# Kernel tuning notes

Measured on AMD Instinct MI355X. Metric: run time of the kernel, lower is better.

## Reference

```python
import jax, jax.numpy as jnp
import numpy as np

B, T, F, H, L, C = 32, 512, 1024, 1024, 2, 2
W_SCALE = 0.03  # small init so tanh stays in its linear-ish range


def setup_inputs() -> dict:
    key = jax.random.key(0)
    ks = jax.random.split(key, 12)
    inp = {
        "x": jax.random.normal(ks[0], (B, T, F), dtype=jnp.float32),
        "h0": jax.random.normal(ks[1], (L, B, H), dtype=jnp.float32),
        # layer 0 (input size F)
        "W_ih0": jax.random.normal(ks[2], (H, F), dtype=jnp.float32) * W_SCALE,
        "W_hh0": jax.random.normal(ks[3], (H, H), dtype=jnp.float32) * W_SCALE,
        "b_ih0": jax.random.normal(ks[4], (H,), dtype=jnp.float32) * W_SCALE,
        "b_hh0": jax.random.normal(ks[5], (H,), dtype=jnp.float32) * W_SCALE,
        # layer 1 (input size H)
        "W_ih1": jax.random.normal(ks[6], (H, H), dtype=jnp.float32) * W_SCALE,
        "W_hh1": jax.random.normal(ks[7], (H, H), dtype=jnp.float32) * W_SCALE,
        "b_ih1": jax.random.normal(ks[8], (H,), dtype=jnp.float32) * W_SCALE,
        "b_hh1": jax.random.normal(ks[9], (H,), dtype=jnp.float32) * W_SCALE,
        # classifier Linear(T*H -> C)
        "W_cls": jax.random.normal(ks[10], (C, T * H), dtype=jnp.float32) * 0.001,
        "b_cls": jax.random.normal(ks[11], (C,), dtype=jnp.float32) * 0.001,
    }
    return inp


def _rnn_layer(x_btf, h0_bh, W_ih, W_hh, b_ih, b_hh):
    # PyTorch RNN (tanh): h_t = tanh(x_t W_ih^T + b_ih + h_{t-1} W_hh^T + b_hh)
    # Precompute the input projection for all timesteps (one big GEMM).
    pre = jnp.einsum("btf,hf->bth", x_btf, W_ih) + b_ih + b_hh  # [B,T,H]
    pre_t = jnp.swapaxes(pre, 0, 1)  # [T,B,H] for scan

    def step(h, p):  # h: [B,H], p: [B,H]
        h_new = jnp.tanh(p + h @ W_hh.T)
        return h_new, h_new

    h_last, ys = jax.lax.scan(step, h0_bh, pre_t)
    return jnp.swapaxes(ys, 0, 1), h_last  # [B,T,H], [B,H]


def reference(x, h0, W_ih0, W_hh0, b_ih0, b_hh0, W_ih1, W_hh1, b_ih1, b_hh1, W_cls, b_cls):
    y0, h0_last = _rnn_layer(x, h0[0], W_ih0, W_hh0, b_ih0, b_hh0)
    y1, h1_last = _rnn_layer(y0, h0[1], W_ih1, W_hh1, b_ih1, b_hh1)
    h_n = jnp.stack([h0_last, h1_last], axis=0)  # [L,B,H]
    flat = y1.reshape(y1.shape[0], -1)  # [B, T*H]
    logits = flat @ W_cls.T + b_cls  # Dropout(0.1) is identity at inference
    return logits, h_n
```

## Files before the change

### kernel.cpp

```cpp
#include <hip/hip_runtime.h>
#include <math.h>

typedef float f4 __attribute__((ext_vector_type(4)));
typedef short bf16x8 __attribute__((ext_vector_type(8)));
typedef unsigned u32x2 __attribute__((ext_vector_type(2)));
typedef unsigned u32x4 __attribute__((ext_vector_type(4)));

#define NT 512

#define H00 0
#define H01 32768
#define H10 65536
#define H11 98304
#define PLOG 131072
#define FLAGS 135168
#define WSW  139520
#define XBF  4333824

__device__ __forceinline__ unsigned pack_bf16(float lo, float hi) {
  unsigned u;
  asm volatile("v_cvt_pk_bf16_f32 %0, %1, %2" : "=v"(u) : "v"(lo), "v"(hi));
  return u;
}
__device__ __forceinline__ float bflo(unsigned d) { return __uint_as_float(d << 16); }
__device__ __forceinline__ float bfhi(unsigned d) { return __uint_as_float(d & 0xffff0000u); }
__device__ __forceinline__ void st_cohf(float* p, float v) {
  __hip_atomic_store(p, v, __ATOMIC_RELAXED, __HIP_MEMORY_SCOPE_AGENT);
}
__device__ __forceinline__ void st_cohu(unsigned* p, unsigned v) {
  __hip_atomic_store(p, v, __ATOMIC_RELAXED, __HIP_MEMORY_SCOPE_AGENT);
}
__device__ __forceinline__ unsigned ld_flag(const unsigned* p) {
  return __hip_atomic_load(p, __ATOMIC_RELAXED, __HIP_MEMORY_SCOPE_AGENT);
}

__device__ __forceinline__ void split8(const f4 v0, const f4 v1, u32x4& hi, u32x4& lo) {
  float h_[8] = {v0[0], v0[1], v0[2], v0[3], v1[0], v1[1], v1[2], v1[3]};
  #pragma unroll
  for (int e = 0; e < 4; ++e) hi[e] = pack_bf16(h_[2*e], h_[2*e+1]);
  float r[8];
  #pragma unroll
  for (int e = 0; e < 4; ++e) {
    r[2*e]   = h_[2*e]   - bflo(hi[e]);
    r[2*e+1] = h_[2*e+1] - bfhi(hi[e]);
  }
  #pragma unroll
  for (int e = 0; e < 4; ++e) lo[e] = pack_bf16(r[2*e], r[2*e+1]);
}

__global__ __launch_bounds__(128) void wconv_kernel(
    const float* __restrict__ W0, const float* __restrict__ W1,
    const float* __restrict__ W2, const float* __restrict__ W3,
    float* __restrict__ ws) {
  const int mat = blockIdx.x >> 10;
  const int j = blockIdx.x & 1023;
  const int kc = threadIdx.x;
  const float* Wm = (mat == 0) ? W0 : (mat == 1) ? W1 : (mat == 2) ? W2 : W3;
  const f4* src = (const f4*)(Wm + (size_t)j * 1024 + kc * 8);
  f4 v0 = src[0], v1 = src[1];
  u32x4 hi, lo;
  split8(v0, v1, hi, lo);
  u32x4* dst = (u32x4*)((f4*)ws + (WSW >> 2));
  size_t base = (size_t)(mat * 2) * 131072 + (j >> 4) * 2048 + kc * 16 + (j & 15);
  dst[base] = hi;
  dst[base + 131072] = lo;
}

__global__ __launch_bounds__(128) void xconv_kernel(const float* __restrict__ x,
                                                    float* __restrict__ ws) {
  const int t = blockIdx.x;
  const int kc = threadIdx.x;
  u32x4* dst = (u32x4*)((f4*)ws + (XBF >> 2)) + (size_t)t * 4096;
  for (int b = 0; b < 32; ++b) {
    const f4* src = (const f4*)(x + ((size_t)b * NT + t) * 1024 + kc * 8);
    f4 v0 = src[0], v1 = src[1];
    u32x4 p;
    #pragma unroll
    for (int e = 0; e < 4; ++e)
      p[e] = pack_bf16(e < 2 ? v0[2*e] : v1[2*e-4], e < 2 ? v0[2*e+1] : v1[2*e-3]);
    dst[(size_t)kc * 32 + b] = p;
  }
}

__global__ __launch_bounds__(256) void hinit_kernel(const float* __restrict__ h0,
                                                    float* __restrict__ ws) {
  int g = blockIdx.x * 256 + threadIdx.x;
  int l = g >> 12, b = (g >> 7) & 31, kc = g & 127;
  const f4* src = (const f4*)(h0 + (size_t)l * 32768 + b * 1024 + kc * 8);
  f4 v0 = src[0], v1 = src[1];
  u32x4 hi, lo;
  split8(v0, v1, hi, lo);
  u32x4* d = (u32x4*)((unsigned*)ws + (l ? H11 : H00));
  d[(size_t)kc * 32 + b] = hi;
  d[4096 + (size_t)kc * 32 + b] = lo;
  if (g < 4352) ((unsigned*)ws)[FLAGS + g] = 0u;
}

#define LDG(dst, ptr) \
  asm volatile("global_load_dwordx4 %0, %1, off sc0" : "=v"(dst) : "v"(ptr))
#define MFMA(a, b, c) __builtin_amdgcn_mfma_f32_16x16x32_bf16(a, b, c, 0, 0, 0)
#define BC(v) __builtin_bit_cast(bf16x8, v)

#define KT_L0(kt, N)                                                     \
  asm volatile("s_waitcnt vmcnt(" #N ")");                               \
  __builtin_amdgcn_sched_barrier(0xF4);                                  \
  {                                                                      \
    const int ci = (ch0 + kt * 4) * 16 + jl;                             \
    bf16x8 a0 = w4b[ci], a1 = w4b[2048 + ci], a2 = w4b[4096 + ci];       \
    bf16x8 vh = BC(bh[kt]), vl = BC(bl[kt]), vx = BC(bx[kt]);            \
    cr = MFMA(a0, vh, cr); cr = MFMA(a0, vl, cr); cr = MFMA(a1, vh, cr); \
    cp = MFMA(a2, vx, cp);                                               \
  }

#define KT_L1(kt, N)                                                     \
  asm volatile("s_waitcnt vmcnt(" #N ")");                               \
  __builtin_amdgcn_sched_barrier(0xF4);                                  \
  {                                                                      \
    const int ci = (ch0 + kt * 4) * 16 + jl;                             \
    bf16x8 a0 = w4b[ci], a1 = w4b[2048 + ci];                            \
    bf16x8 a2 = w4b[4096 + ci], a3 = w4b[6144 + ci];                     \
    bf16x8 h0h = BC(bh[kt]), h0l = BC(bl[kt]);                           \
    bf16x8 h1h = BC(ch_[kt]), h1l = BC(cl_[kt]);                         \
    cr = MFMA(a0, h0h, cr); cr = MFMA(a0, h0l, cr); cr = MFMA(a1, h0h, cr); \
    cr = MFMA(a2, h1h, cr); cr = MFMA(a2, h1l, cr); cr = MFMA(a3, h1h, cr); \
  }

#define KT_PRE(kt, N)                                                    \
  asm volatile("s_waitcnt vmcnt(" #N ")");                               \
  __builtin_amdgcn_sched_barrier(0xF4);                                  \
  {                                                                      \
    const int ci = (ch0 + kt * 4) * 16 + jl;                             \
    bf16x8 a2 = w4b[4096 + ci];                                          \
    cp = MFMA(a2, BC(bx[kt]), cp);                                       \
  }

__global__ __launch_bounds__(512, 1) void rnn_kernel(
    const float* __restrict__ bih0, const float* __restrict__ bhh0,
    const float* __restrict__ bih1, const float* __restrict__ bhh1,
    const float* __restrict__ Wcls, const float* __restrict__ bcls,
    float* __restrict__ out, float* ws) {
  extern __shared__ float smem[];
  f4* w4 = (f4*)smem;
  bf16x8* w4b = (bf16x8*)smem;
  f4* partR = w4 + 8192;
  f4* partP = w4 + 8704;
  float* prebuf = smem + 36864;

  const int bid = blockIdx.x, tid = threadIdx.x;
  const bool isL1 = bid >= 64;
  const int jsl = bid & 63;
  const int l = tid & 63, w = tid >> 6;
  const int nt = w & 1, ks = w >> 1;
  const int jl = l & 15;
  const int bcol = nt * 16 + (l & 15);
  const int ch0 = ks * 32 + (l >> 4);

  unsigned* flags = (unsigned*)ws + FLAGS;
  unsigned* relc = flags + 4096;
  const f4* wsf4 = (const f4*)ws;

  {
    const int m0 = isL1 ? 2 : 0;
    for (int i = tid; i < 8192; i += 512) {
      const int slot = i >> 11, idx = i & 2047;
      const int mat = m0 + (slot >> 1), part = slot & 1;
      w4[i] = wsf4[(WSW >> 2) + (size_t)(mat * 2 + part) * 131072 +
                   jsl * 2048 + idx];
    }
  }

  const int rr = tid & 63, ntr = (tid >> 6) & 1;
  const int b_r = ntr * 16 + (rr & 15);
  const int jg = rr >> 4;
  const int jcol0 = jsl * 16 + jg * 4;
  f4 biasv = (f4)0.f;
  if (tid < 128) {
    f4 bi = isL1 ? *(const f4*)(bih1 + jcol0) : *(const f4*)(bih0 + jcol0);
    f4 bh2 = isL1 ? *(const f4*)(bhh1 + jcol0) : *(const f4*)(bhh0 + jcol0);
    biasv = bi + bh2;
  }
  float lg0 = 0.f, lg1 = 0.f;
  __syncthreads();

  if (!isL1) {
    f4 bx[8];
    const f4* px = wsf4 + (XBF >> 2) + ch0 * 32 + bcol;
    LDG(bx[0], px);            LDG(bx[1], px + 128);
    LDG(bx[2], px + 256);      LDG(bx[3], px + 384);
    LDG(bx[4], px + 512);      LDG(bx[5], px + 640);
    LDG(bx[6], px + 768);      LDG(bx[7], px + 896);
    f4 cp = (f4)0.f;
    KT_PRE(0, 7) KT_PRE(1, 6) KT_PRE(2, 5) KT_PRE(3, 4)
    KT_PRE(4, 3) KT_PRE(5, 2) KT_PRE(6, 1) KT_PRE(7, 0)
    partP[(ks * 2 + nt) * 64 + l] = cp;
    __syncthreads();
    if (tid >= 128 && tid < 256) {
      f4 sum = partP[ntr * 64 + rr] + partP[(2 + ntr) * 64 + rr] +
               partP[(4 + ntr) * 64 + rr] + partP[(6 + ntr) * 64 + rr];
      #pragma unroll
      for (int e = 0; e < 4; ++e)
        prebuf[(jg * 4 + e) * 32 + b_r] = sum[e];
    }
    __syncthreads();
  }

  for (int s = 0; s <= NT; ++s) {
    if (bid == 0) {
      if (tid < 128) {
        const unsigned* fp = &flags[tid * 32];
        while (ld_flag(fp) < (unsigned)s) {}
      }
      __syncthreads();
      if (tid < 8) st_cohu(&relc[tid * 32], (unsigned)s);
    } else {
      if (tid == 0) {
        const unsigned* rxp = &relc[(bid & 7) * 32];
        while (ld_flag(rxp) < (unsigned)s) {}
      }
      __syncthreads();
    }
    __builtin_amdgcn_sched_barrier(0);

    const int rp = s & 1;
    const bool act = isL1 ? (s >= 1) : (s < NT);

    f4 wc0 = (f4)0.f, wc1 = (f4)0.f;
    if (isL1 && tid < 128 && s >= 1) {
      wc0 = *(const f4*)(Wcls + (size_t)(s - 1) * 1024 + jcol0);
      wc1 = *(const f4*)(Wcls + (size_t)524288 + (size_t)(s - 1) * 1024 + jcol0);
    }

    if (act) {
      if (!isL1) {
        const int tn = (s + 1 < NT) ? (s + 1) : (NT - 1);
        const f4* ph = wsf4 + ((rp ? H01 : H00) >> 2) + ch0 * 32 + bcol;
        const f4* pl = ph + 4096;
        const f4* px = wsf4 + (XBF >> 2) + (size_t)tn * 4096 + ch0 * 32 + bcol;
        f4 bh[8], bl[8], bx[8];
        LDG(bh[0], ph);       LDG(bl[0], pl);       LDG(bx[0], px);
        LDG(bh[1], ph + 128); LDG(bl[1], pl + 128); LDG(bx[1], px + 128);
        LDG(bh[2], ph + 256); LDG(bl[2], pl + 256); LDG(bx[2], px + 256);
        LDG(bh[3], ph + 384); LDG(bl[3], pl + 384); LDG(bx[3], px + 384);
        LDG(bh[4], ph + 512); LDG(bl[4], pl + 512); LDG(bx[4], px + 512);
        LDG(bh[5], ph + 640); LDG(bl[5], pl + 640); LDG(bx[5], px + 640);
        LDG(bh[6], ph + 768); LDG(bl[6], pl + 768); LDG(bx[6], px + 768);
        LDG(bh[7], ph + 896); LDG(bl[7], pl + 896); LDG(bx[7], px + 896);
        f4 cr = (f4)0.f, cp = (f4)0.f;
        KT_L0(0, 21) KT_L0(1, 18) KT_L0(2, 15) KT_L0(3, 12)
        KT_L0(4, 9)  KT_L0(5, 6)  KT_L0(6, 3)  KT_L0(7, 0)
        partR[(ks * 2 + nt) * 64 + l] = cr;
        partP[(ks * 2 + nt) * 64 + l] = cp;
      } else {
        const f4* ph = wsf4 + ((rp ? H01 : H00) >> 2) + ch0 * 32 + bcol;
        const f4* pl = ph + 4096;
        const f4* qh = wsf4 + ((rp ? H11 : H10) >> 2) + ch0 * 32 + bcol;
        const f4* ql = qh + 4096;
        f4 bh[8], bl[8], ch_[8], cl_[8];
        LDG(bh[0], ph);       LDG(bl[0], pl);       LDG(ch_[0], qh);       LDG(cl_[0], ql);
        LDG(bh[1], ph + 128); LDG(bl[1], pl + 128); LDG(ch_[1], qh + 128); LDG(cl_[1], ql + 128);
        LDG(bh[2], ph + 256); LDG(bl[2], pl + 256); LDG(ch_[2], qh + 256); LDG(cl_[2], ql + 256);
        LDG(bh[3], ph + 384); LDG(bl[3], pl + 384); LDG(ch_[3], qh + 384); LDG(cl_[3], ql + 384);
        LDG(bh[4], ph + 512); LDG(bl[4], pl + 512); LDG(ch_[4], qh + 512); LDG(cl_[4], ql + 512);
        LDG(bh[5], ph + 640); LDG(bl[5], pl + 640); LDG(ch_[5], qh + 640); LDG(cl_[5], ql + 640);
        LDG(bh[6], ph + 768); LDG(bl[6], pl + 768); LDG(ch_[6], qh + 768); LDG(cl_[6], ql + 768);
        LDG(bh[7], ph + 896); LDG(bl[7], pl + 896); LDG(ch_[7], qh + 896); LDG(cl_[7], ql + 896);
        f4 cr = (f4)0.f;
        KT_L1(0, 28) KT_L1(1, 24) KT_L1(2, 20) KT_L1(3, 16)
        KT_L1(4, 12) KT_L1(5, 8)  KT_L1(6, 4)  KT_L1(7, 0)
        partR[(ks * 2 + nt) * 64 + l] = cr;
      }
      __syncthreads();

      if (tid < 128) {
        f4 sum = partR[ntr * 64 + rr] + partR[(2 + ntr) * 64 + rr] +
                 partR[(4 + ntr) * 64 + rr] + partR[(6 + ntr) * 64 + rr];
        float h_[4];
        #pragma unroll
        for (int e = 0; e < 4; ++e) {
          float v = sum[e] + biasv[e];
          if (!isL1) v += prebuf[rp * 512 + (jg * 4 + e) * 32 + b_r];
          h_[e] = tanhf(v);
        }
        unsigned hi0 = pack_bf16(h_[0], h_[1]), hi1 = pack_bf16(h_[2], h_[3]);
        float r0 = h_[0] - bflo(hi0), r1 = h_[1] - bfhi(hi0);
        float r2 = h_[2] - bflo(hi1), r3 = h_[3] - bfhi(hi1);
        unsigned lo0 = pack_bf16(r0, r1), lo1 = pack_bf16(r2, r3);
        u32x2 hp; hp[0] = hi0; hp[1] = hi1;
        u32x2 lp; lp[0] = lo0; lp[1] = lo1;
        unsigned dstb = isL1 ? (rp ? H10 : H11) : (rp ? H00 : H01);
        unsigned* dp = (unsigned*)ws + dstb + ((jcol0 >> 3) * 32 + b_r) * 4 +
                       ((jcol0 >> 1) & 3);
        asm volatile("global_store_dwordx2 %0, %1, off sc0 sc1" ::"v"(dp), "v"(hp) : "memory");
        asm volatile("global_store_dwordx2 %0, %1, off sc0 sc1" ::"v"(dp + 16384), "v"(lp) : "memory");
        if (isL1) {
          lg0 += h_[0]*wc0[0] + h_[1]*wc0[1] + h_[2]*wc0[2] + h_[3]*wc0[3];
          lg1 += h_[0]*wc1[0] + h_[1]*wc1[1] + h_[2]*wc1[2] + h_[3]*wc1[3];
          if (s == NT) {
            f4 o; o[0]=h_[0]; o[1]=h_[1]; o[2]=h_[2]; o[3]=h_[3];
            *(f4*)(out + 64 + 32768 + (size_t)b_r * 1024 + jcol0) = o;
          }
        } else if (s == NT - 1) {
          f4 o; o[0]=h_[0]; o[1]=h_[1]; o[2]=h_[2]; o[3]=h_[3];
          *(f4*)(out + 64 + (size_t)b_r * 1024 + jcol0) = o;
        }
      } else if (tid < 256 && !isL1) {
        f4 sum = partP[ntr * 64 + rr] + partP[(2 + ntr) * 64 + rr] +
                 partP[(4 + ntr) * 64 + rr] + partP[(6 + ntr) * 64 + rr];
        #pragma unroll
        for (int e = 0; e < 4; ++e)
          prebuf[(rp ^ 1) * 512 + (jg * 4 + e) * 32 + b_r] = sum[e];
      }
    }
    asm volatile("s_waitcnt vmcnt(0)");
    __syncthreads();
    if (tid == 0) st_cohu(&flags[bid * 32], (unsigned)(s + 1));
  }

  if (isL1) {
    float* lgred = smem + 36864;
    if (tid < 128) {
      lgred[jg * 32 + b_r] = lg0;
      lgred[128 + jg * 32 + b_r] = lg1;
    }
    __syncthreads();
    if (tid < 64) {
      const int c = tid >> 5, bb = tid & 31;
      float v = 0.f;
      #pragma unroll
      for (int g2 = 0; g2 < 4; ++g2) v += lgred[c * 128 + g2 * 32 + bb];
      st_cohf(&ws[PLOG + (size_t)(bid - 64) * 64 + c * 32 + bb], v);
    }
    __syncthreads();
    if (tid == 0) st_cohu(&flags[bid * 32], 600u);
  } else if (bid == 0) {
    if (tid < 64) {
      const unsigned* fp = &flags[(64 + tid) * 32];
      while (ld_flag(fp) < 600u) {}
    }
    __syncthreads();
    __builtin_amdgcn_sched_barrier(0);
    float* lgred = smem + 36864;
    if (tid < 256) {
      const int g2 = tid >> 6, pair = tid & 63;
      float v = 0.f;
      for (int blk = g2; blk < 64; blk += 4)
        v += __hip_atomic_load(&ws[PLOG + (size_t)blk * 64 + pair],
                               __ATOMIC_RELAXED, __HIP_MEMORY_SCOPE_AGENT);
      lgred[tid] = v;
    }
    __syncthreads();
    if (tid < 64) {
      float s2 = bcls[tid >> 5];
      #pragma unroll
      for (int g2 = 0; g2 < 4; ++g2) s2 += lgred[g2 * 64 + tid];
      out[(size_t)(tid & 31) * 2 + (tid >> 5)] = s2;
    }
  }
}

extern "C" void kernel_launch(void* const* d_in, const int* in_sizes, int n_in,
                              void* d_out, int out_size, void* d_ws, size_t ws_size,
                              hipStream_t stream) {
  const float* x    = (const float*)d_in[0];
  const float* h0   = (const float*)d_in[1];
  const float* Wih0 = (const float*)d_in[2];
  const float* Whh0 = (const float*)d_in[3];
  const float* bih0 = (const float*)d_in[4];
  const float* bhh0 = (const float*)d_in[5];
  const float* Wih1 = (const float*)d_in[6];
  const float* Whh1 = (const float*)d_in[7];
  const float* bih1 = (const float*)d_in[8];
  const float* bhh1 = (const float*)d_in[9];
  const float* Wcls = (const float*)d_in[10];
  const float* bcls = (const float*)d_in[11];
  float* out = (float*)d_out;
  float* ws  = (float*)d_ws;

  hipFuncSetAttribute((const void*)rnn_kernel,
                      hipFuncAttributeMaxDynamicSharedMemorySize, 151552);

  hipLaunchKernelGGL(wconv_kernel, dim3(4096), dim3(128), 0, stream,
                     Whh0, Wih0, Wih1, Whh1, ws);
  hipLaunchKernelGGL(xconv_kernel, dim3(512), dim3(128), 0, stream, x, ws);
  hipLaunchKernelGGL(hinit_kernel, dim3(32), dim3(256), 0, stream, h0, ws);

  void* args[] = { (void*)&bih0, (void*)&bhh0, (void*)&bih1, (void*)&bhh1,
                   (void*)&Wcls, (void*)&bcls, (void*)&out, (void*)&ws };
  hipLaunchCooperativeKernel((void*)rnn_kernel, dim3(128), dim3(512), args,
                             151552, stream);
}
```

Baseline: 2.702 ms.

## Decouple RNN layers with per-layer flags and ring-buffered hidden states

Replaces the global per-step barrier (block 0 gathering all flags and broadcasting a release counter) with separate per-layer flag arrays, so layer-0 blocks wait only on their peers and on layer 1 lagging at most three steps. Layer-0 hidden states go into a four-slot ring, and layer 1 now computes its input projection from layer-0 output with split-bf16 MFMAs instead of fusing that work into one step. The x projection for the next step is moved after the flag publish to take it off the critical path. This lets the two layers run pipelined rather than in lockstep, at the cost of more flag polling and a more complex dependency scheme.

```diff
diff --git a/kernel.cpp b/kernel.cpp
--- a/kernel.cpp
+++ b/kernel.cpp
@@ -8,14 +8,12 @@
 
 #define NT 512
 
-#define H00 0
-#define H01 32768
-#define H10 65536
-#define H11 98304
-#define PLOG 131072
-#define FLAGS 135168
-#define WSW  139520
-#define XBF  4333824
+#define H0R 0
+#define H1R 131072
+#define PLOG 196608
+#define FLAGS 200704
+#define WSW 204800
+#define XBF 4399104
 
 __device__ __forceinline__ unsigned pack_bf16(float lo, float hi) {
   unsigned u;
@@ -30,8 +28,8 @@
 __device__ __forceinline__ void st_cohu(unsigned* p, unsigned v) {
   __hip_atomic_store(p, v, __ATOMIC_RELAXED, __HIP_MEMORY_SCOPE_AGENT);
 }
-__device__ __forceinline__ unsigned ld_flag(const unsigned* p) {
-  return __hip_atomic_load(p, __ATOMIC_RELAXED, __HIP_MEMORY_SCOPE_AGENT);
+__device__ __forceinline__ int ld_flag(const unsigned* p) {
+  return (int)__hip_atomic_load(p, __ATOMIC_RELAXED, __HIP_MEMORY_SCOPE_AGENT);
 }
 
 __device__ __forceinline__ void split8(const f4 v0, const f4 v1, u32x4& hi, u32x4& lo) {
@@ -90,10 +88,11 @@
   f4 v0 = src[0], v1 = src[1];
   u32x4 hi, lo;
   split8(v0, v1, hi, lo);
-  u32x4* d = (u32x4*)((unsigned*)ws + (l ? H11 : H00));
+  unsigned base = l ? (H1R + 32768) : (H0R + 3 * 32768);
+  u32x4* d = (u32x4*)((unsigned*)ws + base);
   d[(size_t)kc * 32 + b] = hi;
   d[4096 + (size_t)kc * 32 + b] = lo;
-  if (g < 4352) ((unsigned*)ws)[FLAGS + g] = 0u;
+  if (g < 4096) ((unsigned*)ws)[FLAGS + g] = 0u;
 }
 
 #define LDG(dst, ptr) \
@@ -101,38 +100,44 @@
 #define MFMA(a, b, c) __builtin_amdgcn_mfma_f32_16x16x32_bf16(a, b, c, 0, 0, 0)
 #define BC(v) __builtin_bit_cast(bf16x8, v)
 
-#define KT_L0(kt, N)                                                     \
-  asm volatile("s_waitcnt vmcnt(" #N ")");                               \
-  __builtin_amdgcn_sched_barrier(0xF4);                                  \
-  {                                                                      \
-    const int ci = (ch0 + kt * 4) * 16 + jl;                             \
-    bf16x8 a0 = w4b[ci], a1 = w4b[2048 + ci], a2 = w4b[4096 + ci];       \
-    bf16x8 vh = BC(bh[kt]), vl = BC(bl[kt]), vx = BC(bx[kt]);            \
-    cr = MFMA(a0, vh, cr); cr = MFMA(a0, vl, cr); cr = MFMA(a1, vh, cr); \
-    cp = MFMA(a2, vx, cp);                                               \
-  }
-
-#define KT_L1(kt, N)                                                     \
-  asm volatile("s_waitcnt vmcnt(" #N ")");                               \
-  __builtin_amdgcn_sched_barrier(0xF4);                                  \
-  {                                                                      \
-    const int ci = (ch0 + kt * 4) * 16 + jl;                             \
-    bf16x8 a0 = w4b[ci], a1 = w4b[2048 + ci];                            \
-    bf16x8 a2 = w4b[4096 + ci], a3 = w4b[6144 + ci];                     \
-    bf16x8 h0h = BC(bh[kt]), h0l = BC(bl[kt]);                           \
-    bf16x8 h1h = BC(ch_[kt]), h1l = BC(cl_[kt]);                         \
-    cr = MFMA(a0, h0h, cr); cr = MFMA(a0, h0l, cr); cr = MFMA(a1, h0h, cr); \
-    cr = MFMA(a2, h1h, cr); cr = MFMA(a2, h1l, cr); cr = MFMA(a3, h1h, cr); \
-  }
-
-#define KT_PRE(kt, N)                                                    \
-  asm volatile("s_waitcnt vmcnt(" #N ")");                               \
-  __builtin_amdgcn_sched_barrier(0xF4);                                  \
-  {                                                                      \
-    const int ci = (ch0 + kt * 4) * 16 + jl;                             \
-    bf16x8 a2 = w4b[4096 + ci];                                          \
-    cp = MFMA(a2, BC(bx[kt]), cp);                                       \
-  }
+#define KT_M(kt, N)                                                       \
+  asm volatile("s_waitcnt vmcnt(" #N ")");                                \
+  __builtin_amdgcn_sched_barrier(0xF4);                                   \
+  {                                                                       \
+    const int ci = (ch0 + kt * 4) * 16 + jl;                              \
+    bf16x8 a0 = w4b[ci], a1 = w4b[2048 + ci];                             \
+    bf16x8 vh = BC(bh[kt]), vl = BC(bl[kt]);                              \
+    cr = MFMA(a0, vh, cr); cr = MFMA(a0, vl, cr); cr = MFMA(a1, vh, cr);  \
+  }
+
+#define KT_G(kt, N)                                                       \
+  asm volatile("s_waitcnt vmcnt(" #N ")");                                \
+  __builtin_amdgcn_sched_barrier(0xF4);                                   \
+  {                                                                       \
+    const int ci = (ch0 + kt * 4) * 16 + jl;                              \
+    bf16x8 a2 = w4b[4096 + ci], a3 = w4b[6144 + ci];                      \
+    bf16x8 vh = BC(gh[kt]), vl = BC(gl[kt]);                              \
+    cp = MFMA(a2, vh, cp); cp = MFMA(a2, vl, cp); cp = MFMA(a3, vh, cp);  \
+  }
+
+#define KT_X(kt, N)                                                       \
+  asm volatile("s_waitcnt vmcnt(" #N ")");                                \
+  __builtin_amdgcn_sched_barrier(0xF4);                                   \
+  {                                                                       \
+    const int ci = (ch0 + kt * 4) * 16 + jl;                              \
+    bf16x8 a2 = w4b[4096 + ci];                                           \
+    cp = MFMA(a2, BC(bx[kt]), cp);                                        \
+  }
+
+#define LD16(A, B, pa, pb)                                                \
+  LDG(A[0], pa);       LDG(B[0], pb);                                     \
+  LDG(A[1], pa + 128); LDG(B[1], pb + 128);                               \
+  LDG(A[2], pa + 256); LDG(B[2], pb + 256);                               \
+  LDG(A[3], pa + 384); LDG(B[3], pb + 384);                               \
+  LDG(A[4], pa + 512); LDG(B[4], pb + 512);                               \
+  LDG(A[5], pa + 640); LDG(B[5], pb + 640);                               \
+  LDG(A[6], pa + 768); LDG(B[6], pb + 768);                               \
+  LDG(A[7], pa + 896); LDG(B[7], pb + 896);
 
 __global__ __launch_bounds__(512, 1) void rnn_kernel(
     const float* __restrict__ bih0, const float* __restrict__ bhh0,
@@ -155,17 +160,16 @@
   const int bcol = nt * 16 + (l & 15);
   const int ch0 = ks * 32 + (l >> 4);
 
-  unsigned* flags = (unsigned*)ws + FLAGS;
-  unsigned* relc = flags + 4096;
+  unsigned* flag0 = (unsigned*)ws + FLAGS;
+  unsigned* flag1 = flag0 + 64 * 32;
   const f4* wsf4 = (const f4*)ws;
 
   {
-    const int m0 = isL1 ? 2 : 0;
-    for (int i = tid; i < 8192; i += 512) {
+    const int nent = isL1 ? 8192 : 6144;
+    for (int i = tid; i < nent; i += 512) {
       const int slot = i >> 11, idx = i & 2047;
-      const int mat = m0 + (slot >> 1), part = slot & 1;
-      w4[i] = wsf4[(WSW >> 2) + (size_t)(mat * 2 + part) * 131072 +
-                   jsl * 2048 + idx];
+      const int region = isL1 ? (slot < 2 ? 6 + slot : 2 + slot) : slot;
+      w4[i] = wsf4[(WSW >> 2) + (size_t)region * 131072 + jsl * 2048 + idx];
     }
   }
 
@@ -185,90 +189,54 @@
   if (!isL1) {
     f4 bx[8];
     const f4* px = wsf4 + (XBF >> 2) + ch0 * 32 + bcol;
-    LDG(bx[0], px);            LDG(bx[1], px + 128);
-    LDG(bx[2], px + 256);      LDG(bx[3], px + 384);
-    LDG(bx[4], px + 512);      LDG(bx[5], px + 640);
-    LDG(bx[6], px + 768);      LDG(bx[7], px + 896);
+    LDG(bx[0], px);       LDG(bx[1], px + 128);
+    LDG(bx[2], px + 256); LDG(bx[3], px + 384);
+    LDG(bx[4], px + 512); LDG(bx[5], px + 640);
+    LDG(bx[6], px + 768); LDG(bx[7], px + 896);
     f4 cp = (f4)0.f;
-    KT_PRE(0, 7) KT_PRE(1, 6) KT_PRE(2, 5) KT_PRE(3, 4)
-    KT_PRE(4, 3) KT_PRE(5, 2) KT_PRE(6, 1) KT_PRE(7, 0)
+    KT_X(0, 7) KT_X(1, 6) KT_X(2, 5) KT_X(3, 4)
+    KT_X(4, 3) KT_X(5, 2) KT_X(6, 1) KT_X(7, 0)
     partP[(ks * 2 + nt) * 64 + l] = cp;
-    __syncthreads();
-    if (tid >= 128 && tid < 256) {
-      f4 sum = partP[ntr * 64 + rr] + partP[(2 + ntr) * 64 + rr] +
-               partP[(4 + ntr) * 64 + rr] + partP[(6 + ntr) * 64 + rr];
-      #pragma unroll
-      for (int e = 0; e < 4; ++e)
-        prebuf[(jg * 4 + e) * 32 + b_r] = sum[e];
-    }
-    __syncthreads();
-  }
-
-  for (int s = 0; s <= NT; ++s) {
-    if (bid == 0) {
-      if (tid < 128) {
-        const unsigned* fp = &flags[tid * 32];
-        while (ld_flag(fp) < (unsigned)s) {}
-      }
-      __syncthreads();
-      if (tid < 8) st_cohu(&relc[tid * 32], (unsigned)s);
-    } else {
-      if (tid == 0) {
-        const unsigned* rxp = &relc[(bid & 7) * 32];
-        while (ld_flag(rxp) < (unsigned)s) {}
-      }
-      __syncthreads();
-    }
+  } else {
+    if (tid < 64) { while (ld_flag(&flag0[tid * 32]) < 1) {} }
+    __syncthreads();
     __builtin_amdgcn_sched_barrier(0);
-
-    const int rp = s & 1;
-    const bool act = isL1 ? (s >= 1) : (s < NT);
-
-    f4 wc0 = (f4)0.f, wc1 = (f4)0.f;
-    if (isL1 && tid < 128 && s >= 1) {
-      wc0 = *(const f4*)(Wcls + (size_t)(s - 1) * 1024 + jcol0);
-      wc1 = *(const f4*)(Wcls + (size_t)524288 + (size_t)(s - 1) * 1024 + jcol0);
-    }
-
-    if (act) {
-      if (!isL1) {
-        const int tn = (s + 1 < NT) ? (s + 1) : (NT - 1);
-        const f4* ph = wsf4 + ((rp ? H01 : H00) >> 2) + ch0 * 32 + bcol;
-        const f4* pl = ph + 4096;
-        const f4* px = wsf4 + (XBF >> 2) + (size_t)tn * 4096 + ch0 * 32 + bcol;
-        f4 bh[8], bl[8], bx[8];
-        LDG(bh[0], ph);       LDG(bl[0], pl);       LDG(bx[0], px);
-        LDG(bh[1], ph + 128); LDG(bl[1], pl + 128); LDG(bx[1], px + 128);
-        LDG(bh[2], ph + 256); LDG(bl[2], pl + 256); LDG(bx[2], px + 256);
-        LDG(bh[3], ph + 384); LDG(bl[3], pl + 384); LDG(bx[3], px + 384);
-        LDG(bh[4], ph + 512); LDG(bl[4], pl + 512); LDG(bx[4], px + 512);
-        LDG(bh[5], ph + 640); LDG(bl[5], pl + 640); LDG(bx[5], px + 640);
-        LDG(bh[6], ph + 768); LDG(bl[6], pl + 768); LDG(bx[6], px + 768);
-        LDG(bh[7], ph + 896); LDG(bl[7], pl + 896); LDG(bx[7], px + 896);
-        f4 cr = (f4)0.f, cp = (f4)0.f;
-        KT_L0(0, 21) KT_L0(1, 18) KT_L0(2, 15) KT_L0(3, 12)
-        KT_L0(4, 9)  KT_L0(5, 6)  KT_L0(6, 3)  KT_L0(7, 0)
-        partR[(ks * 2 + nt) * 64 + l] = cr;
-        partP[(ks * 2 + nt) * 64 + l] = cp;
-      } else {
-        const f4* ph = wsf4 + ((rp ? H01 : H00) >> 2) + ch0 * 32 + bcol;
-        const f4* pl = ph + 4096;
-        const f4* qh = wsf4 + ((rp ? H11 : H10) >> 2) + ch0 * 32 + bcol;
-        const f4* ql = qh + 4096;
-        f4 bh[8], bl[8], ch_[8], cl_[8];
-        LDG(bh[0], ph);       LDG(bl[0], pl);       LDG(ch_[0], qh);       LDG(cl_[0], ql);
-        LDG(bh[1], ph + 128); LDG(bl[1], pl + 128); LDG(ch_[1], qh + 128); LDG(cl_[1], ql + 128);
-        LDG(bh[2], ph + 256); LDG(bl[2], pl + 256); LDG(ch_[2], qh + 256); LDG(cl_[2], ql + 256);
-        LDG(bh[3], ph + 384); LDG(bl[3], pl + 384); LDG(ch_[3], qh + 384); LDG(cl_[3], ql + 384);
-        LDG(bh[4], ph + 512); LDG(bl[4], pl + 512); LDG(ch_[4], qh + 512); LDG(cl_[4], ql + 512);
-        LDG(bh[5], ph + 640); LDG(bl[5], pl + 640); LDG(ch_[5], qh + 640); LDG(cl_[5], ql + 640);
-        LDG(bh[6], ph + 768); LDG(bl[6], pl + 768); LDG(ch_[6], qh + 768); LDG(cl_[6], ql + 768);
-        LDG(bh[7], ph + 896); LDG(bl[7], pl + 896); LDG(ch_[7], qh + 896); LDG(cl_[7], ql + 896);
-        f4 cr = (f4)0.f;
-        KT_L1(0, 28) KT_L1(1, 24) KT_L1(2, 20) KT_L1(3, 16)
-        KT_L1(4, 12) KT_L1(5, 8)  KT_L1(6, 4)  KT_L1(7, 0)
-        partR[(ks * 2 + nt) * 64 + l] = cr;
-      }
+    const f4* gph = wsf4 + (H0R >> 2) + ch0 * 32 + bcol;
+    const f4* gpl = gph + 4096;
+    f4 gh[8], gl[8];
+    LD16(gh, gl, gph, gpl)
+    f4 cp = (f4)0.f;
+    KT_G(0, 14) KT_G(1, 12) KT_G(2, 10) KT_G(3, 8)
+    KT_G(4, 6)  KT_G(5, 4)  KT_G(6, 2)  KT_G(7, 0)
+    partP[(ks * 2 + nt) * 64 + l] = cp;
+  }
+  __syncthreads();
+  if (tid >= 128 && tid < 256) {
+    f4 sum = partP[ntr * 64 + rr] + partP[(2 + ntr) * 64 + rr] +
+             partP[(4 + ntr) * 64 + rr] + partP[(6 + ntr) * 64 + rr];
+    #pragma unroll
+    for (int e = 0; e < 4; ++e) prebuf[(jg * 4 + e) * 32 + b_r] = sum[e];
+  }
+
+  if (!isL1) {
+    for (int s = 0; s < NT; ++s) {
+      if (tid < 64) { while (ld_flag(&flag0[tid * 32]) < s) {} }
+      else if (tid < 128) {
+        const int bound = s - 3;
+        while (ld_flag(&flag1[(tid - 64) * 32]) < bound) {}
+      }
+      __syncthreads();
+      __builtin_amdgcn_sched_barrier(0);
+      const int pp = s & 1;
+
+      const f4* ph = wsf4 + (H0R >> 2) + ((s + 3) & 3) * 8192 + ch0 * 32 + bcol;
+      const f4* pl = ph + 4096;
+      f4 bh[8], bl[8];
+      LD16(bh, bl, ph, pl)
+      f4 cr = (f4)0.f;
+      KT_M(0, 14) KT_M(1, 12) KT_M(2, 10) KT_M(3, 8)
+      KT_M(4, 6)  KT_M(5, 4)  KT_M(6, 2)  KT_M(7, 0)
+      partR[(ks * 2 + nt) * 64 + l] = cr;
       __syncthreads();
 
       if (tid < 128) {
@@ -276,48 +244,122 @@
                  partR[(4 + ntr) * 64 + rr] + partR[(6 + ntr) * 64 + rr];
         float h_[4];
         #pragma unroll
-        for (int e = 0; e < 4; ++e) {
-          float v = sum[e] + biasv[e];
-          if (!isL1) v += prebuf[rp * 512 + (jg * 4 + e) * 32 + b_r];
-          h_[e] = tanhf(v);
-        }
+        for (int e = 0; e < 4; ++e)
+          h_[e] = tanhf(sum[e] + biasv[e] + prebuf[pp * 512 + (jg * 4 + e) * 32 + b_r]);
         unsigned hi0 = pack_bf16(h_[0], h_[1]), hi1 = pack_bf16(h_[2], h_[3]);
-        float r0 = h_[0] - bflo(hi0), r1 = h_[1] - bfhi(hi0);
-        float r2 = h_[2] - bflo(hi1), r3 = h_[3] - bfhi(hi1);
-        unsigned lo0 = pack_bf16(r0, r1), lo1 = pack_bf16(r2, r3);
+        unsigned lo0 = pack_bf16(h_[0] - bflo(hi0), h_[1] - bfhi(hi0));
+        unsigned lo1 = pack_bf16(h_[2] - bflo(hi1), h_[3] - bfhi(hi1));
         u32x2 hp; hp[0] = hi0; hp[1] = hi1;
         u32x2 lp; lp[0] = lo0; lp[1] = lo1;
-        unsigned dstb = isL1 ? (rp ? H10 : H11) : (rp ? H00 : H01);
-        unsigned* dp = (unsigned*)ws + dstb + ((jcol0 >> 3) * 32 + b_r) * 4 +
-                       ((jcol0 >> 1) & 3);
+        unsigned* dp = (unsigned*)ws + H0R + (s & 3) * 32768 +
+                       ((jcol0 >> 3) * 32 + b_r) * 4 + ((jcol0 >> 1) & 3);
         asm volatile("global_store_dwordx2 %0, %1, off sc0 sc1" ::"v"(dp), "v"(hp) : "memory");
         asm volatile("global_store_dwordx2 %0, %1, off sc0 sc1" ::"v"(dp + 16384), "v"(lp) : "memory");
-        if (isL1) {
-          lg0 += h_[0]*wc0[0] + h_[1]*wc0[1] + h_[2]*wc0[2] + h_[3]*wc0[3];
-          lg1 += h_[0]*wc1[0] + h_[1]*wc1[1] + h_[2]*wc1[2] + h_[3]*wc1[3];
-          if (s == NT) {
-            f4 o; o[0]=h_[0]; o[1]=h_[1]; o[2]=h_[2]; o[3]=h_[3];
-            *(f4*)(out + 64 + 32768 + (size_t)b_r * 1024 + jcol0) = o;
-          }
-        } else if (s == NT - 1) {
+        if (s == NT - 1) {
           f4 o; o[0]=h_[0]; o[1]=h_[1]; o[2]=h_[2]; o[3]=h_[3];
           *(f4*)(out + 64 + (size_t)b_r * 1024 + jcol0) = o;
         }
-      } else if (tid < 256 && !isL1) {
-        f4 sum = partP[ntr * 64 + rr] + partP[(2 + ntr) * 64 + rr] +
-                 partP[(4 + ntr) * 64 + rr] + partP[(6 + ntr) * 64 + rr];
+      }
+      asm volatile("s_waitcnt vmcnt(0)");
+      __syncthreads();
+      if (tid == 0) st_cohu(&flag0[bid * 32], (unsigned)(s + 1));
+
+      if (s < NT - 1) {
+        const f4* px = wsf4 + (XBF >> 2) + (size_t)(s + 1) * 4096 + ch0 * 32 + bcol;
+        f4 bx[8];
+        LDG(bx[0], px);       LDG(bx[1], px + 128);
+        LDG(bx[2], px + 256); LDG(bx[3], px + 384);
+        LDG(bx[4], px + 512); LDG(bx[5], px + 640);
+        LDG(bx[6], px + 768); LDG(bx[7], px + 896);
+        f4 cp = (f4)0.f;
+        KT_X(0, 7) KT_X(1, 6) KT_X(2, 5) KT_X(3, 4)
+        KT_X(4, 3) KT_X(5, 2) KT_X(6, 1) KT_X(7, 0)
+        partP[(ks * 2 + nt) * 64 + l] = cp;
+        __syncthreads();
+        if (tid >= 128 && tid < 256) {
+          f4 sum = partP[ntr * 64 + rr] + partP[(2 + ntr) * 64 + rr] +
+                   partP[(4 + ntr) * 64 + rr] + partP[(6 + ntr) * 64 + rr];
+          #pragma unroll
+          for (int e = 0; e < 4; ++e)
+            prebuf[(pp ^ 1) * 512 + (jg * 4 + e) * 32 + b_r] = sum[e];
+        }
+      }
+    }
+  } else {
+    for (int t = 0; t < NT; ++t) {
+      if (tid < 64) { while (ld_flag(&flag1[tid * 32]) < t) {} }
+      __syncthreads();
+      __builtin_amdgcn_sched_barrier(0);
+      const int pp = t & 1;
+
+      f4 wc0 = (f4)0.f, wc1 = (f4)0.f;
+      if (tid < 128) {
+        wc0 = *(const f4*)(Wcls + (size_t)t * 1024 + jcol0);
+        wc1 = *(const f4*)(Wcls + (size_t)524288 + (size_t)t * 1024 + jcol0);
+      }
+      __builtin_amdgcn_sched_barrier(0);
+
+      const f4* ph = wsf4 + (H1R >> 2) + ((t + 1) & 1) * 8192 + ch0 * 32 + bcol;
+      const f4* pl = ph + 4096;
+      f4 bh[8], bl[8];
+      LD16(bh, bl, ph, pl)
+      f4 cr = (f4)0.f;
+      KT_M(0, 14) KT_M(1, 12) KT_M(2, 10) KT_M(3, 8)
+      KT_M(4, 6)  KT_M(5, 4)  KT_M(6, 2)  KT_M(7, 0)
+      partR[(ks * 2 + nt) * 64 + l] = cr;
+      __syncthreads();
+
+      if (tid < 128) {
+        f4 sum = partR[ntr * 64 + rr] + partR[(2 + ntr) * 64 + rr] +
+                 partR[(4 + ntr) * 64 + rr] + partR[(6 + ntr) * 64 + rr];
+        float h_[4];
         #pragma unroll
         for (int e = 0; e < 4; ++e)
-          prebuf[(rp ^ 1) * 512 + (jg * 4 + e) * 32 + b_r] = sum[e];
-      }
-    }
-    asm volatile("s_waitcnt vmcnt(0)");
-    __syncthreads();
-    if (tid == 0) st_cohu(&flags[bid * 32], (unsigned)(s + 1));
-  }
-
-  if (isL1) {
-    float* lgred = smem + 36864;
+          h_[e] = tanhf(sum[e] + biasv[e] + prebuf[pp * 512 + (jg * 4 + e) * 32 + b_r]);
+        unsigned hi0 = pack_bf16(h_[0], h_[1]), hi1 = pack_bf16(h_[2], h_[3]);
+        unsigned lo0 = pack_bf16(h_[0] - bflo(hi0), h_[1] - bfhi(hi0));
+        unsigned lo1 = pack_bf16(h_[2] - bflo(hi1), h_[3] - bfhi(hi1));
+        u32x2 hp; hp[0] = hi0; hp[1] = hi1;
+        u32x2 lp; lp[0] = lo0; lp[1] = lo1;
+        unsigned* dp = (unsigned*)ws + H1R + (t & 1) * 32768 +
+                       ((jcol0 >> 3) * 32 + b_r) * 4 + ((jcol0 >> 1) & 3);
+        asm volatile("global_store_dwordx2 %0, %1, off sc0 sc1" ::"v"(dp), "v"(hp) : "memory");
+        asm volatile("global_store_dwordx2 %0, %1, off sc0 sc1" ::"v"(dp + 16384), "v"(lp) : "memory");
+        lg0 += h_[0]*wc0[0] + h_[1]*wc0[1] + h_[2]*wc0[2] + h_[3]*wc0[3];
+        lg1 += h_[0]*wc1[0] + h_[1]*wc1[1] + h_[2]*wc1[2] + h_[3]*wc1[3];
+        if (t == NT - 1) {
+          f4 o; o[0]=h_[0]; o[1]=h_[1]; o[2]=h_[2]; o[3]=h_[3];
+          *(f4*)(out + 64 + 32768 + (size_t)b_r * 1024 + jcol0) = o;
+        }
+      }
+      asm volatile("s_waitcnt vmcnt(0)");
+      __syncthreads();
+      if (tid == 0) st_cohu(&flag1[(bid - 64) * 32], (unsigned)(t + 1));
+
+      if (t < NT - 1) {
+        if (tid < 64) { while (ld_flag(&flag0[tid * 32]) < t + 2) {} }
+        __syncthreads();
+        __builtin_amdgcn_sched_barrier(0);
+        const f4* gph = wsf4 + (H0R >> 2) + ((t + 1) & 3) * 8192 + ch0 * 32 + bcol;
+        const f4* gpl = gph + 4096;
+        f4 gh[8], gl[8];
+        LD16(gh, gl, gph, gpl)
+        f4 cp = (f4)0.f;
+        KT_G(0, 14) KT_G(1, 12) KT_G(2, 10) KT_G(3, 8)
+        KT_G(4, 6)  KT_G(5, 4)  KT_G(6, 2)  KT_G(7, 0)
+        partP[(ks * 2 + nt) * 64 + l] = cp;
+        __syncthreads();
+        if (tid >= 128 && tid < 256) {
+          f4 sum = partP[ntr * 64 + rr] + partP[(2 + ntr) * 64 + rr] +
+                   partP[(4 + ntr) * 64 + rr] + partP[(6 + ntr) * 64 + rr];
+          #pragma unroll
+          for (int e = 0; e < 4; ++e)
+            prebuf[(pp ^ 1) * 512 + (jg * 4 + e) * 32 + b_r] = sum[e];
+        }
+      }
+    }
+    float* lgred = (float*)(w4 + 8192);
+    __syncthreads();
     if (tid < 128) {
       lgred[jg * 32 + b_r] = lg0;
       lgred[128 + jg * 32 + b_r] = lg1;
@@ -331,15 +373,14 @@
       st_cohf(&ws[PLOG + (size_t)(bid - 64) * 64 + c * 32 + bb], v);
     }
     __syncthreads();
-    if (tid == 0) st_cohu(&flags[bid * 32], 600u);
-  } else if (bid == 0) {
-    if (tid < 64) {
-      const unsigned* fp = &flags[(64 + tid) * 32];
-      while (ld_flag(fp) < 600u) {}
-    }
+    if (tid == 0) st_cohu(&flag1[(bid - 64) * 32], 600u);
+  }
+
+  if (bid == 0) {
+    if (tid < 64) { while (ld_flag(&flag1[tid * 32]) < 600) {} }
     __syncthreads();
     __builtin_amdgcn_sched_barrier(0);
-    float* lgred = smem + 36864;
+    float* lgred = (float*)(w4 + 8192);
     if (tid < 256) {
       const int g2 = tid >> 6, pair = tid & 63;
       float v = 0.f;
```

New measurement: 2.417 ms. 10.6% less time.
